# Optimization experiments

Hardware: AMD Instinct MI355X
Metric: run time of the kernel (lower is better)

The kernel has to match this reference:

```python
import jax, jax.numpy as jnp
import numpy as np

N_NODES = 100000
N_EDGES = 1600000
F_IN, F_HID, F_OUT = 128, 256, 128


def setup_inputs() -> dict:
    key = jax.random.key(0)
    ks = jax.random.split(key, 9)
    x = jax.random.normal(ks[0], (N_NODES, F_IN), dtype=jnp.float32)
    edge_src = jax.random.randint(ks[1], (N_EDGES,), 0, N_NODES, dtype=jnp.int32)
    edge_dst = jax.random.randint(ks[2], (N_EDGES,), 0, N_NODES, dtype=jnp.int32)
    s1 = 1.0 / np.sqrt(F_IN)
    s2 = 1.0 / np.sqrt(F_HID)
    W_self1 = jax.random.uniform(ks[3], (F_IN, F_HID), jnp.float32, -s1, s1)
    W_neigh1 = jax.random.uniform(ks[4], (F_IN, F_HID), jnp.float32, -s1, s1)
    b1 = jnp.zeros((F_HID,), jnp.float32)
    W_self2 = jax.random.uniform(ks[5], (F_HID, F_OUT), jnp.float32, -s2, s2)
    W_neigh2 = jax.random.uniform(ks[6], (F_HID, F_OUT), jnp.float32, -s2, s2)
    b2 = jnp.zeros((F_OUT,), jnp.float32)
    return {"x": x, "edge_src": edge_src, "edge_dst": edge_dst,
            "W_self1": W_self1, "W_neigh1": W_neigh1, "b1": b1,
            "W_self2": W_self2, "W_neigh2": W_neigh2, "b2": b2}


def _sage_mean(h, src, dst, W_self, W_neigh, b):
    # mean-aggregate neighbor features onto dst nodes (DGL SAGEConv 'mean')
    deg = jax.ops.segment_sum(jnp.ones_like(src, dtype=h.dtype), dst,
                              num_segments=N_NODES)
    neigh_sum = jax.ops.segment_sum(h[src], dst, num_segments=N_NODES)
    neigh = neigh_sum / jnp.maximum(deg, 1.0)[:, None]
    return h @ W_self + neigh @ W_neigh + b


def reference(x, edge_src, edge_dst, W_self1, W_neigh1, b1, W_self2, W_neigh2, b2):
    h = _sage_mean(x, edge_src, edge_dst, W_self1, W_neigh1, b1)
    h = jax.nn.sigmoid(h)
    h = _sage_mean(h, edge_src, edge_dst, W_self2, W_neigh2, b2)
    return h
```

## Files before the change

### kernel.cpp

```cpp
#include <hip/hip_runtime.h>
#include <hip/hip_bf16.h>

#define N_NODES 100000
#define N_EDGES 1600000
#define F_IN 128
#define F_HID 256
#define F_OUT 128

typedef unsigned short ushort_t;
typedef __attribute__((ext_vector_type(4))) float f32x4;
typedef __attribute__((ext_vector_type(8))) short bf16x8;

#define GAS __attribute__((address_space(1)))
#define LAS __attribute__((address_space(3)))

__device__ __forceinline__ float bf2f(ushort_t u) {
    unsigned int x = ((unsigned int)u) << 16;
    return __builtin_bit_cast(float, x);
}
__device__ __forceinline__ ushort_t f2bf(float f) {
    unsigned int x = __builtin_bit_cast(unsigned int, f);
    unsigned int r = (x + 0x7fffu + ((x >> 16) & 1u)) >> 16;
    return (ushort_t)r;
}

#define NBUCK ((N_NODES + 255) >> 8)
#define CHUNK 4096

__global__ __launch_bounds__(256) void bucket_count_kernel(
    const int* __restrict__ dst, int* __restrict__ bucket_cnt, int n) {
    __shared__ int hist[NBUCK];
    int tid = threadIdx.x;
    int e0 = blockIdx.x * CHUNK;
    int cnt = n - e0; if (cnt > CHUNK) cnt = CHUNK;
    for (int b = tid; b < NBUCK; b += 256) hist[b] = 0;
    __syncthreads();
    for (int i = tid; i < cnt; i += 256) {
        int d = __builtin_nontemporal_load(dst + e0 + i);
        atomicAdd(&hist[d >> 8], 1);
    }
    __syncthreads();
    for (int b = tid; b < NBUCK; b += 256)
        if (hist[b]) atomicAdd(&bucket_cnt[b], hist[b]);
}

__global__ __launch_bounds__(512) void bucket_scan_kernel(
    const int* __restrict__ bucket_cnt, int* __restrict__ bbase,
    int* __restrict__ bcursor, int* __restrict__ rowptr) {
    __shared__ int tmp[512];
    int tid = threadIdx.x;
    int v = (tid < NBUCK) ? bucket_cnt[tid] : 0;
    tmp[tid] = v;
    __syncthreads();
#pragma unroll
    for (int off = 1; off < 512; off <<= 1) {
        int t = (tid >= off) ? tmp[tid - off] : 0;
        __syncthreads();
        tmp[tid] += t;
        __syncthreads();
    }
    if (tid < NBUCK) {
        int base = tmp[tid] - v;
        bbase[tid] = base;
        bcursor[tid] = base;
    }
    if (tid == 0) {
        bbase[NBUCK] = N_EDGES;
        rowptr[N_NODES] = N_EDGES;
    }
}

__global__ __launch_bounds__(256) void bin_edges_kernel(
    const int* __restrict__ src, const int* __restrict__ dst,
    int* __restrict__ bcursor, unsigned int* __restrict__ pairs, int n) {
    __shared__ int sdst[CHUNK];
    __shared__ int ssrc[CHUNK];
    __shared__ int hist[NBUCK];
    __shared__ int resv[NBUCK];
    int tid = threadIdx.x;
    int e0 = blockIdx.x * CHUNK;
    int cnt = n - e0; if (cnt > CHUNK) cnt = CHUNK;
    for (int b = tid; b < NBUCK; b += 256) hist[b] = 0;
    __syncthreads();
    for (int i = tid; i < cnt; i += 256) {
        int d = __builtin_nontemporal_load(dst + e0 + i);
        int s = __builtin_nontemporal_load(src + e0 + i);
        sdst[i] = d;
        ssrc[i] = s;
        atomicAdd(&hist[d >> 8], 1);
    }
    __syncthreads();
    for (int b = tid; b < NBUCK; b += 256) {
        int h = hist[b];
        resv[b] = h ? atomicAdd(&bcursor[b], h) : 0;
        hist[b] = 0;
    }
    __syncthreads();
    for (int i = tid; i < cnt; i += 256) {
        int d = sdst[i], s = ssrc[i];
        int b = d >> 8;
        int off = atomicAdd(&hist[b], 1);
        pairs[resv[b] + off] = ((unsigned)(d & 255) << 17) | (unsigned)s;
    }
}

__global__ __launch_bounds__(256) void sort_bucket_kernel(
    const unsigned int* __restrict__ pairs, const int* __restrict__ bbase,
    int* __restrict__ rowptr, float* __restrict__ invdeg,
    int* __restrict__ csr_src, int nNodes) {
    __shared__ int lcnt[256];
    __shared__ int lrp[256];
    int tid = threadIdx.x;
    int base = blockIdx.x << 8;
    int nn = nNodes - base; if (nn > 256) nn = 256;
    lcnt[tid] = 0;
    __syncthreads();
    int e0 = bbase[blockIdx.x], e1 = bbase[blockIdx.x + 1];
    for (int i = e0 + tid; i < e1; i += 256)
        atomicAdd(&lcnt[pairs[i] >> 17], 1);
    __syncthreads();
    int v = lcnt[tid];
    lrp[tid] = v;
    __syncthreads();
#pragma unroll
    for (int off = 1; off < 256; off <<= 1) {
        int t = (tid >= off) ? lrp[tid - off] : 0;
        __syncthreads();
        lrp[tid] += t;
        __syncthreads();
    }
    lcnt[tid] = 0;
    lrp[tid] = lrp[tid] - v + e0;
    if (tid < nn) {
        rowptr[base + tid] = lrp[tid];
        invdeg[base + tid] = 1.0f / fmaxf((float)v, 1.0f);
    }
    __syncthreads();
    for (int i = e0 + tid; i < e1; i += 256) {
        unsigned pv = pairs[i];
        int j = (int)(pv >> 17);
        int off = atomicAdd(&lcnt[j], 1);
        csr_src[lrp[j] + off] = (int)(pv & 0x1FFFFu);
    }
}

__global__ __launch_bounds__(256) void convert_x_kernel(const float* __restrict__ x,
                                                        ushort_t* __restrict__ xb, int n4) {
    int i = blockIdx.x * 256 + threadIdx.x;
    if (i >= n4) return;
    int e = i * 4;
    f32x4 v = __builtin_nontemporal_load((const f32x4*)(x + e));
    ushort4 o;
    o.x = f2bf(v.x); o.y = f2bf(v.y); o.z = f2bf(v.z); o.w = f2bf(v.w);
    *(ushort4*)(xb + e) = o;
}

__global__ __launch_bounds__(256) void wtransK_kernel(const float* __restrict__ W1,
                                                      const float* __restrict__ W2,
                                                      ushort_t* __restrict__ Wt,
                                                      int Kx, int Ktot, int N) {
    int i = blockIdx.x * 256 + threadIdx.x;
    if (i >= N * Ktot) return;
    int n = i / Ktot, k = i - n * Ktot;
    float v = (k < Kx) ? W1[(size_t)k * N + n] : W2[(size_t)(k - Kx) * N + n];
    Wt[(size_t)n * Ktot + k] = f2bf(v);
}

__global__ __launch_bounds__(256) void wtransN_kernel(const float* __restrict__ Wa,
                                                      const float* __restrict__ Wb,
                                                      ushort_t* __restrict__ Wt,
                                                      int K, int Nh) {
    int i = blockIdx.x * 256 + threadIdx.x;
    if (i >= 2 * Nh * K) return;
    int n = i / K, k = i - n * K;
    const float* W = (n < Nh) ? Wa : Wb;
    int nn = (n < Nh) ? n : n - Nh;
    Wt[(size_t)n * K + k] = f2bf(W[(size_t)k * Nh + nn]);
}

#define ACC8(arr, v)                                                \
    arr[0] += bf2f((ushort_t)((v).x & 0xffffu));                    \
    arr[1] += bf2f((ushort_t)((v).x >> 16));                        \
    arr[2] += bf2f((ushort_t)((v).y & 0xffffu));                    \
    arr[3] += bf2f((ushort_t)((v).y >> 16));                        \
    arr[4] += bf2f((ushort_t)((v).z & 0xffffu));                    \
    arr[5] += bf2f((ushort_t)((v).z >> 16));                        \
    arr[6] += bf2f((ushort_t)((v).w & 0xffffu));                    \
    arr[7] += bf2f((ushort_t)((v).w >> 16));

template <int MODE>
__global__ __launch_bounds__(256) void gather2_kernel(
    const ushort_t* __restrict__ H,
    const int* __restrict__ rowptr,
    const int* __restrict__ csr_src,
    const float* __restrict__ invdeg,
    const ushort_t* __restrict__ uself,
    const float* __restrict__ bias,
    void* __restrict__ outp,
    int nNodes, int totWaves) {
    int lane = threadIdx.x & 63;
    int wv = blockIdx.x * 4 + (threadIdx.x >> 6);
    int grp = lane >> 4, sub = lane & 15;
    const size_t cofs = (size_t)sub * 8;
    int pair = wv;
    if (pair * 2 >= nNodes) return;
    int r0 = rowptr[pair * 2];
    int r1 = rowptr[pair * 2 + 1];
    int r2 = rowptr[pair * 2 + 2];
    while (true) {
        int npair = pair + totWaves;
        bool hasNext = (npair * 2 < nNodes);
        int n0 = 0, n1 = 0, n2 = 0;
        if (hasNext) {
            n0 = rowptr[npair * 2];
            n1 = rowptr[npair * 2 + 1];
            n2 = rowptr[npair * 2 + 2];
        }
        int nodeA = pair * 2;
        int sA = r0, eA = r1, sB = r1, eB = r2;
        int cA = sA < N_EDGES ? sA : N_EDGES - 1;
        int cB = sB < N_EDGES ? sB : N_EDGES - 1;
        float accA[8] = {}, accB[8] = {};
        for (int ea = sA + grp, eb = sB + grp; ea < eA || eb < eB; ea += 16, eb += 16) {
            bool pa0 = ea < eA, pa1 = ea + 4 < eA, pa2 = ea + 8 < eA, pa3 = ea + 12 < eA;
            bool pb0 = eb < eB, pb1 = eb + 4 < eB, pb2 = eb + 8 < eB, pb3 = eb + 12 < eB;
            int ja0 = pa0 ? ea : cA, ja1 = pa1 ? ea + 4 : cA;
            int ja2 = pa2 ? ea + 8 : cA, ja3 = pa3 ? ea + 12 : cA;
            int jb0 = pb0 ? eb : cB, jb1 = pb1 ? eb + 4 : cB;
            int jb2 = pb2 ? eb + 8 : cB, jb3 = pb3 ? eb + 12 : cB;
            int sa0 = csr_src[ja0], sa1 = csr_src[ja1];
            int sa2 = csr_src[ja2], sa3 = csr_src[ja3];
            int sb0 = csr_src[jb0], sb1 = csr_src[jb1];
            int sb2 = csr_src[jb2], sb3 = csr_src[jb3];
            uint4 va0 = *(const uint4*)(H + (size_t)sa0 * 128 + cofs);
            uint4 va1 = *(const uint4*)(H + (size_t)sa1 * 128 + cofs);
            uint4 va2 = *(const uint4*)(H + (size_t)sa2 * 128 + cofs);
            uint4 va3 = *(const uint4*)(H + (size_t)sa3 * 128 + cofs);
            uint4 vb0 = *(const uint4*)(H + (size_t)sb0 * 128 + cofs);
            uint4 vb1 = *(const uint4*)(H + (size_t)sb1 * 128 + cofs);
            uint4 vb2 = *(const uint4*)(H + (size_t)sb2 * 128 + cofs);
            uint4 vb3 = *(const uint4*)(H + (size_t)sb3 * 128 + cofs);
            if (pa0) { ACC8(accA, va0); }
            if (pa1) { ACC8(accA, va1); }
            if (pa2) { ACC8(accA, va2); }
            if (pa3) { ACC8(accA, va3); }
            if (pb0) { ACC8(accB, vb0); }
            if (pb1) { ACC8(accB, vb1); }
            if (pb2) { ACC8(accB, vb2); }
            if (pb3) { ACC8(accB, vb3); }
        }
#pragma unroll
        for (int j = 0; j < 8; ++j) {
            accA[j] += __shfl_xor(accA[j], 16);
            accA[j] += __shfl_xor(accA[j], 32);
            accB[j] += __shfl_xor(accB[j], 16);
            accB[j] += __shfl_xor(accB[j], 32);
        }
        if (grp == 0) {
            int nodeB = nodeA + 1;
            float scA = invdeg[nodeA];
            float scB = (nodeB < nNodes) ? invdeg[nodeB] : 1.0f;
            if (MODE == 0) {
                uint4 o;
                o.x = (unsigned)f2bf(accA[0] * scA) | ((unsigned)f2bf(accA[1] * scA) << 16);
                o.y = (unsigned)f2bf(accA[2] * scA) | ((unsigned)f2bf(accA[3] * scA) << 16);
                o.z = (unsigned)f2bf(accA[4] * scA) | ((unsigned)f2bf(accA[5] * scA) << 16);
                o.w = (unsigned)f2bf(accA[6] * scA) | ((unsigned)f2bf(accA[7] * scA) << 16);
                *(uint4*)((ushort_t*)outp + (size_t)nodeA * 128 + cofs) = o;
                if (nodeB < nNodes) {
                    uint4 p2;
                    p2.x = (unsigned)f2bf(accB[0] * scB) | ((unsigned)f2bf(accB[1] * scB) << 16);
                    p2.y = (unsigned)f2bf(accB[2] * scB) | ((unsigned)f2bf(accB[3] * scB) << 16);
                    p2.z = (unsigned)f2bf(accB[4] * scB) | ((unsigned)f2bf(accB[5] * scB) << 16);
                    p2.w = (unsigned)f2bf(accB[6] * scB) | ((unsigned)f2bf(accB[7] * scB) << 16);
                    *(uint4*)((ushort_t*)outp + (size_t)nodeB * 128 + cofs) = p2;
                }
            } else {
                uint4 us = *(const uint4*)(uself + (size_t)nodeA * 128 + cofs);
                f32x4 o0, o1;
                o0.x = accA[0] * scA + bf2f((ushort_t)(us.x & 0xffffu)) + bias[cofs + 0];
                o0.y = accA[1] * scA + bf2f((ushort_t)(us.x >> 16)) + bias[cofs + 1];
                o0.z = accA[2] * scA + bf2f((ushort_t)(us.y & 0xffffu)) + bias[cofs + 2];
                o0.w = accA[3] * scA + bf2f((ushort_t)(us.y >> 16)) + bias[cofs + 3];
                o1.x = accA[4] * scA + bf2f((ushort_t)(us.z & 0xffffu)) + bias[cofs + 4];
                o1.y = accA[5] * scA + bf2f((ushort_t)(us.z >> 16)) + bias[cofs + 5];
                o1.z = accA[6] * scA + bf2f((ushort_t)(us.w & 0xffffu)) + bias[cofs + 6];
                o1.w = accA[7] * scA + bf2f((ushort_t)(us.w >> 16)) + bias[cofs + 7];
                float* op = (float*)outp + (size_t)nodeA * 128 + cofs;
                __builtin_nontemporal_store(o0, (f32x4*)op);
                __builtin_nontemporal_store(o1, (f32x4*)(op + 4));
                if (nodeB < nNodes) {
                    uint4 u2 = *(const uint4*)(uself + (size_t)nodeB * 128 + cofs);
                    f32x4 q0, q1;
                    q0.x = accB[0] * scB + bf2f((ushort_t)(u2.x & 0xffffu)) + bias[cofs + 0];
                    q0.y = accB[1] * scB + bf2f((ushort_t)(u2.x >> 16)) + bias[cofs + 1];
                    q0.z = accB[2] * scB + bf2f((ushort_t)(u2.y & 0xffffu)) + bias[cofs + 2];
                    q0.w = accB[3] * scB + bf2f((ushort_t)(u2.y >> 16)) + bias[cofs + 3];
                    q1.x = accB[4] * scB + bf2f((ushort_t)(u2.z & 0xffffu)) + bias[cofs + 4];
                    q1.y = accB[5] * scB + bf2f((ushort_t)(u2.z >> 16)) + bias[cofs + 5];
                    q1.z = accB[6] * scB + bf2f((ushort_t)(u2.w & 0xffffu)) + bias[cofs + 6];
                    q1.w = accB[7] * scB + bf2f((ushort_t)(u2.w >> 16)) + bias[cofs + 7];
                    float* oq = (float*)outp + (size_t)nodeB * 128 + cofs;
                    __builtin_nontemporal_store(q0, (f32x4*)oq);
                    __builtin_nontemporal_store(q1, (f32x4*)(oq + 4));
                }
            }
        }
        if (!hasNext) break;
        pair = npair; r0 = n0; r1 = n1; r2 = n2;
    }
}

__global__ __launch_bounds__(512) void gemm_mfma_kernel(
    const ushort_t* __restrict__ A1, int lda1,
    const ushort_t* __restrict__ A2, int lda2, int Kx,
    const ushort_t* __restrict__ Bt,
    const float* __restrict__ bias,
    ushort_t* __restrict__ CoutA, int ldcA,
    ushort_t* __restrict__ CoutB, int ldcB,
    int M, int mode) {
    __shared__ ushort_t shmem[2 * 128 * 32 + 2 * 256 * 32];
    ushort_t* Asb[2] = {shmem, shmem + 4096};
    ushort_t* Bsb[2] = {shmem + 8192, shmem + 16384};
    int tid = threadIdx.x;
    int lane = tid & 63, wid = tid >> 6;
    int l15 = lane & 15, kgrp = lane >> 4;
    int bm = blockIdx.x * 128;
    int wr = (wid >> 2) * 64, wc = (wid & 3) * 64;

    auto stage = [&](int buf, int t) {
        int k0 = t * 32;
        const ushort_t* Ap = (k0 < Kx) ? A1 : A2;
        int lda = (k0 < Kx) ? lda1 : lda2;
        int kk0 = (k0 < Kx) ? k0 : k0 - Kx;
        {
            int row = wid * 16 + (lane >> 2);
            int scol = ((lane & 3) ^ (row & 3)) << 3;
            int ar = bm + row; if (ar > M - 1) ar = M - 1;
            __builtin_amdgcn_global_load_lds(
                (const GAS void*)(Ap + (size_t)ar * lda + kk0 + scol),
                (LAS void*)(&Asb[buf][wid * 512]), 16, 0, 0);
        }
#pragma unroll
        for (int t2 = 0; t2 < 2; ++t2) {
            int c = wid * 2 + t2;
            int row = c * 16 + (lane >> 2);
            int scol = ((lane & 3) ^ (row & 3)) << 3;
            __builtin_amdgcn_global_load_lds(
                (const GAS void*)(Bt + (size_t)row * 256 + k0 + scol),
                (LAS void*)(&Bsb[buf][c * 512]), 16, 0, 0);
        }
    };

    f32x4 acc[4][4] = {};

    stage(0, 0);
    __syncthreads();
#pragma unroll
    for (int t = 0; t < 8; ++t) {
        int buf = t & 1;
        if (t < 7) stage(buf ^ 1, t + 1);
        bf16x8 af[4], bfv[4];
#pragma unroll
        for (int mi = 0; mi < 4; ++mi) {
            int row = wr + mi * 16 + l15;
            af[mi] = *(const bf16x8*)(&Asb[buf][row * 32 + ((kgrp ^ (row & 3)) << 3)]);
        }
#pragma unroll
        for (int ni = 0; ni < 4; ++ni) {
            int row = wc + ni * 16 + l15;
            bfv[ni] = *(const bf16x8*)(&Bsb[buf][row * 32 + ((kgrp ^ (row & 3)) << 3)]);
        }
#pragma unroll
        for (int mi = 0; mi < 4; ++mi)
#pragma unroll
            for (int ni = 0; ni < 4; ++ni)
                acc[mi][ni] = __builtin_amdgcn_mfma_f32_16x16x32_bf16(
                    af[mi], bfv[ni], acc[mi][ni], 0, 0, 0);
        __syncthreads();
    }

    ushort_t* my = shmem + wid * 1024;
#pragma unroll
    for (int mi = 0; mi < 4; ++mi) {
#pragma unroll
        for (int ni = 0; ni < 4; ++ni) {
            int gcol = wc + ni * 16 + l15;
#pragma unroll
            for (int r = 0; r < 4; ++r) {
                float v = acc[mi][ni][r];
                if (mode == 0) {
                    v += bias[gcol];
                    v = 1.0f / (1.0f + __expf(-v));
                }
                int lr = kgrp * 4 + r;
                int lc = (ni * 16 + l15) ^ (kgrp << 3);
                my[lr * 64 + lc] = f2bf(v);
            }
        }
#pragma unroll
        for (int it = 0; it < 2; ++it) {
            int r2 = (lane >> 3) + it * 8;
            int swz = ((r2 >> 2) & 3) << 3;
            int c2 = ((lane & 7) << 3) ^ swz;
            bf16x8 vv = *(const bf16x8*)(&my[r2 * 64 + c2]);
            int grow = bm + wr + mi * 16 + r2;
            if (grow < M) {
                int gc = wc + (c2 ^ swz);
                ushort_t* dstp = (gc < 128)
                    ? CoutA + (size_t)grow * ldcA + gc
                    : CoutB + (size_t)grow * ldcB + (gc - 128);
                *(bf16x8*)dstp = vv;
            }
        }
    }
}

extern "C" void kernel_launch(void* const* d_in, const int* in_sizes, int n_in,
                              void* d_out, int out_size, void* d_ws, size_t ws_size,
                              hipStream_t stream) {
    const float* x        = (const float*)d_in[0];
    const int*   src      = (const int*)d_in[1];
    const int*   dst      = (const int*)d_in[2];
    const float* W_self1  = (const float*)d_in[3];
    const float* W_neigh1 = (const float*)d_in[4];
    const float* b1       = (const float*)d_in[5];
    const float* W_self2  = (const float*)d_in[6];
    const float* W_neigh2 = (const float*)d_in[7];
    const float* b2       = (const float*)d_in[8];
    float* out = (float*)d_out;

    char* p = (char*)d_ws;
    auto alloc = [&](size_t bytes) { char* r = p; p += (bytes + 255) & ~(size_t)255; return r; };
    float*    invdeg   = (float*)alloc((size_t)N_NODES * 4);
    ushort_t* xb       = (ushort_t*)alloc((size_t)N_NODES * 128 * 2);
    ushort_t* agg      = (ushort_t*)alloc((size_t)N_NODES * 128 * 2);
    ushort_t* h        = (ushort_t*)alloc((size_t)N_NODES * 256 * 2);
    ushort_t* uself    = (ushort_t*)alloc((size_t)N_NODES * 128 * 2);
    ushort_t* uneigh   = (ushort_t*)alloc((size_t)N_NODES * 128 * 2);
    ushort_t* Wt1      = (ushort_t*)alloc((size_t)256 * 256 * 2);
    ushort_t* Wt2      = (ushort_t*)alloc((size_t)256 * 256 * 2);
    int* rowptr        = (int*)alloc((size_t)(N_NODES + 1) * 4);
    int* bucket_cnt    = (int*)alloc((size_t)NBUCK * 4);
    int* bbase         = (int*)alloc((size_t)(NBUCK + 1) * 4);
    int* bcursor       = (int*)alloc((size_t)NBUCK * 4);
    unsigned int* pairs= (unsigned int*)alloc((size_t)N_EDGES * 4);
    int* csr_src       = (int*)alloc((size_t)N_EDGES * 4);

    convert_x_kernel<<<(N_NODES * F_IN / 4 + 255) / 256, 256, 0, stream>>>(
        x, xb, N_NODES * F_IN / 4);
    wtransK_kernel<<<(256 * 256 + 255) / 256, 256, 0, stream>>>(
        W_self1, W_neigh1, Wt1, 128, 256, 256);
    wtransN_kernel<<<(256 * 256 + 255) / 256, 256, 0, stream>>>(
        W_self2, W_neigh2, Wt2, 256, 128);

    hipMemsetAsync(bucket_cnt, 0, (size_t)NBUCK * sizeof(int), stream);
    bucket_count_kernel<<<(N_EDGES + CHUNK - 1) / CHUNK, 256, 0, stream>>>(
        dst, bucket_cnt, N_EDGES);
    bucket_scan_kernel<<<1, 512, 0, stream>>>(bucket_cnt, bbase, bcursor, rowptr);
    bin_edges_kernel<<<(N_EDGES + CHUNK - 1) / CHUNK, 256, 0, stream>>>(
        src, dst, bcursor, pairs, N_EDGES);
    sort_bucket_kernel<<<NBUCK, 256, 0, stream>>>(
        pairs, bbase, rowptr, invdeg, csr_src, N_NODES);

    const int GATHER_BLOCKS = 2048;
    const int TOT_WAVES = GATHER_BLOCKS * 4;

    gather2_kernel<0><<<GATHER_BLOCKS, 256, 0, stream>>>(
        xb, rowptr, csr_src, invdeg, nullptr, nullptr, agg, N_NODES, TOT_WAVES);
    {
        dim3 grid((N_NODES + 127) / 128);
        gemm_mfma_kernel<<<grid, 512, 0, stream>>>(
            xb, 128, agg, 128, 128, Wt1, b1, h, 256, h + 128, 256, N_NODES, 0);
    }

    {
        dim3 grid((N_NODES + 127) / 128);
        gemm_mfma_kernel<<<grid, 512, 0, stream>>>(
            h, 256, h, 256, 256, Wt2, nullptr, uself, 128, uneigh, 128, N_NODES, 1);
    }
    gather2_kernel<1><<<GATHER_BLOCKS, 256, 0, stream>>>(
        uneigh, rowptr, csr_src, invdeg, uself, b2, out, N_NODES, TOT_WAVES);
}
```

Before: 282.9 us.

## Fuse layer-1 and layer-2 GEMMs keeping hidden activations in LDS

Merges the two MFMA GEMM kernels into one. The sigmoid hidden tile (128x256 bf16) is kept in shared memory and fed straight into the second GEMM against Wt2, which removes the global write and re-read of the h buffer (about 51 MB each way) and one kernel launch. In exchange, shared memory per block grows to roughly 112 KB (64 KB for the hidden tile plus the staging buffers), which lowers occupancy. It also serialises the two GEMM phases inside each block.

```diff
diff --git a/kernel.cpp b/kernel.cpp
--- a/kernel.cpp
+++ b/kernel.cpp
@@ -311,36 +311,37 @@
     }
 }
 
-__global__ __launch_bounds__(512) void gemm_mfma_kernel(
-    const ushort_t* __restrict__ A1, int lda1,
-    const ushort_t* __restrict__ A2, int lda2, int Kx,
-    const ushort_t* __restrict__ Bt,
-    const float* __restrict__ bias,
-    ushort_t* __restrict__ CoutA, int ldcA,
-    ushort_t* __restrict__ CoutB, int ldcB,
-    int M, int mode) {
-    __shared__ ushort_t shmem[2 * 128 * 32 + 2 * 256 * 32];
-    ushort_t* Asb[2] = {shmem, shmem + 4096};
-    ushort_t* Bsb[2] = {shmem + 8192, shmem + 16384};
+__global__ __launch_bounds__(512) void gemm_fused_kernel(
+    const ushort_t* __restrict__ xb,
+    const ushort_t* __restrict__ agg,
+    const ushort_t* __restrict__ Wt1,
+    const float* __restrict__ b1,
+    const ushort_t* __restrict__ Wt2,
+    ushort_t* __restrict__ uself,
+    ushort_t* __restrict__ uneigh,
+    int M) {
+    __shared__ ushort_t hs[128 * 256];
+    __shared__ ushort_t Asb[2][128 * 32];
+    __shared__ ushort_t Bsb[2][256 * 32];
     int tid = threadIdx.x;
     int lane = tid & 63, wid = tid >> 6;
     int l15 = lane & 15, kgrp = lane >> 4;
     int bm = blockIdx.x * 128;
     int wr = (wid >> 2) * 64, wc = (wid & 3) * 64;
 
-    auto stage = [&](int buf, int t) {
+    auto stageA = [&](int buf, int t) {
         int k0 = t * 32;
-        const ushort_t* Ap = (k0 < Kx) ? A1 : A2;
-        int lda = (k0 < Kx) ? lda1 : lda2;
-        int kk0 = (k0 < Kx) ? k0 : k0 - Kx;
-        {
-            int row = wid * 16 + (lane >> 2);
-            int scol = ((lane & 3) ^ (row & 3)) << 3;
-            int ar = bm + row; if (ar > M - 1) ar = M - 1;
-            __builtin_amdgcn_global_load_lds(
-                (const GAS void*)(Ap + (size_t)ar * lda + kk0 + scol),
-                (LAS void*)(&Asb[buf][wid * 512]), 16, 0, 0);
-        }
+        const ushort_t* Ap = (k0 < 128) ? xb : agg;
+        int kk0 = k0 & 127;
+        int row = wid * 16 + (lane >> 2);
+        int scol = ((lane & 3) ^ (row & 3)) << 3;
+        int ar = bm + row; if (ar > M - 1) ar = M - 1;
+        __builtin_amdgcn_global_load_lds(
+            (const GAS void*)(Ap + (size_t)ar * 128 + kk0 + scol),
+            (LAS void*)(&Asb[buf][wid * 512]), 16, 0, 0);
+    };
+    auto stageB = [&](int buf, int t, const ushort_t* Bt) {
+        int k0 = t * 32;
 #pragma unroll
         for (int t2 = 0; t2 < 2; ++t2) {
             int c = wid * 2 + t2;
@@ -354,12 +355,12 @@
 
     f32x4 acc[4][4] = {};
 
-    stage(0, 0);
+    stageA(0, 0); stageB(0, 0, Wt1);
     __syncthreads();
 #pragma unroll
     for (int t = 0; t < 8; ++t) {
         int buf = t & 1;
-        if (t < 7) stage(buf ^ 1, t + 1);
+        if (t < 7) { stageA(buf ^ 1, t + 1); stageB(buf ^ 1, t + 1, Wt1); }
         bf16x8 af[4], bfv[4];
 #pragma unroll
         for (int mi = 0; mi < 4; ++mi) {
@@ -380,22 +381,60 @@
         __syncthreads();
     }
 
-    ushort_t* my = shmem + wid * 1024;
 #pragma unroll
     for (int mi = 0; mi < 4; ++mi) {
 #pragma unroll
         for (int ni = 0; ni < 4; ++ni) {
-            int gcol = wc + ni * 16 + l15;
+            int hcol = wc + ni * 16 + l15;
+            float bv = b1[hcol];
 #pragma unroll
             for (int r = 0; r < 4; ++r) {
-                float v = acc[mi][ni][r];
-                if (mode == 0) {
-                    v += bias[gcol];
-                    v = 1.0f / (1.0f + __expf(-v));
-                }
+                float v = acc[mi][ni][r] + bv;
+                v = 1.0f / (1.0f + __expf(-v));
+                int lr = wr + mi * 16 + kgrp * 4 + r;
+                hs[lr * 256 + (hcol ^ ((lr & 7) << 3))] = f2bf(v);
+                acc[mi][ni][r] = 0.0f;
+            }
+        }
+    }
+    stageB(0, 0, Wt2);
+    __syncthreads();
+#pragma unroll
+    for (int t = 0; t < 8; ++t) {
+        int buf = t & 1;
+        if (t < 7) stageB(buf ^ 1, t + 1, Wt2);
+        int k0 = t * 32;
+        bf16x8 af[4], bfv[4];
+#pragma unroll
+        for (int mi = 0; mi < 4; ++mi) {
+            int row = wr + mi * 16 + l15;
+            int c = k0 + kgrp * 8;
+            af[mi] = *(const bf16x8*)(&hs[row * 256 + (c ^ ((row & 7) << 3))]);
+        }
+#pragma unroll
+        for (int ni = 0; ni < 4; ++ni) {
+            int row = wc + ni * 16 + l15;
+            bfv[ni] = *(const bf16x8*)(&Bsb[buf][row * 32 + ((kgrp ^ (row & 3)) << 3)]);
+        }
+#pragma unroll
+        for (int mi = 0; mi < 4; ++mi)
+#pragma unroll
+            for (int ni = 0; ni < 4; ++ni)
+                acc[mi][ni] = __builtin_amdgcn_mfma_f32_16x16x32_bf16(
+                    af[mi], bfv[ni], acc[mi][ni], 0, 0, 0);
+        __syncthreads();
+    }
+
+    ushort_t* my = ((ushort_t*)Asb) + wid * 1024;
+#pragma unroll
+    for (int mi = 0; mi < 4; ++mi) {
+#pragma unroll
+        for (int ni = 0; ni < 4; ++ni) {
+#pragma unroll
+            for (int r = 0; r < 4; ++r) {
                 int lr = kgrp * 4 + r;
                 int lc = (ni * 16 + l15) ^ (kgrp << 3);
-                my[lr * 64 + lc] = f2bf(v);
+                my[lr * 64 + lc] = f2bf(acc[mi][ni][r]);
             }
         }
 #pragma unroll
@@ -408,8 +447,8 @@
             if (grow < M) {
                 int gc = wc + (c2 ^ swz);
                 ushort_t* dstp = (gc < 128)
-                    ? CoutA + (size_t)grow * ldcA + gc
-                    : CoutB + (size_t)grow * ldcB + (gc - 128);
+                    ? uself + (size_t)grow * 128 + gc
+                    : uneigh + (size_t)grow * 128 + (gc - 128);
                 *(bf16x8*)dstp = vv;
             }
         }
@@ -435,7 +474,6 @@
     float*    invdeg   = (float*)alloc((size_t)N_NODES * 4);
     ushort_t* xb       = (ushort_t*)alloc((size_t)N_NODES * 128 * 2);
     ushort_t* agg      = (ushort_t*)alloc((size_t)N_NODES * 128 * 2);
-    ushort_t* h        = (ushort_t*)alloc((size_t)N_NODES * 256 * 2);
     ushort_t* uself    = (ushort_t*)alloc((size_t)N_NODES * 128 * 2);
     ushort_t* uneigh   = (ushort_t*)alloc((size_t)N_NODES * 128 * 2);
     ushort_t* Wt1      = (ushort_t*)alloc((size_t)256 * 256 * 2);
@@ -470,14 +508,8 @@
         xb, rowptr, csr_src, invdeg, nullptr, nullptr, agg, N_NODES, TOT_WAVES);
     {
         dim3 grid((N_NODES + 127) / 128);
-        gemm_mfma_kernel<<<grid, 512, 0, stream>>>(
-            xb, 128, agg, 128, 128, Wt1, b1, h, 256, h + 128, 256, N_NODES, 0);
-    }
-
-    {
-        dim3 grid((N_NODES + 127) / 128);
-        gemm_mfma_kernel<<<grid, 512, 0, stream>>>(
-            h, 256, h, 256, 256, Wt2, nullptr, uself, 128, uneigh, 128, N_NODES, 1);
+        gemm_fused_kernel<<<grid, 512, 0, stream>>>(
+            xb, agg, Wt1, b1, Wt2, uself, uneigh, N_NODES);
     }
     gather2_kernel<1><<<GATHER_BLOCKS, 256, 0, stream>>>(
         uneigh, rowptr, csr_src, invdeg, uself, b2, out, N_NODES, TOT_WAVES);
```

Result: slower. 289.0 us (+2.1%).
